# Performance work log

Hardware: AMD Instinct MI355X
Metric: run time of the kernel (lower is better)

The kernel has to match this reference:

```python
import jax, jax.numpy as jnp
import numpy as np

P, N, M, B = 5, 30000, 50000, 256
T, C, L, ED, H, EMB, TD, NL = 13, 16, 3, 4, 128, 64, 5, 3
SRC = jnp.repeat(jnp.arange(P), P)  # edge type i = src*P + dst
DST = jnp.tile(jnp.arange(P), P)


def _affine(x, W, b):
    # x: [P, n, i], W: [P, i, o], b: [P, o]
    return jnp.einsum('pni,pio->pno', x, W) + b[:, None, :]


def _lrelu(x, s=0.01):
    return jnp.where(x >= 0, x, s * x)


def _gat(h, W, a_s, a_d, We, a_e, b, edge_index, edge_attr):
    # h: [P, N, H]; per-edge-type GATConv (heads=1, no self loops) then hetero 'max' aggregation
    hs, hd = h[SRC], h[DST]                       # [25, N, H]
    xl = jnp.einsum('enh,ehf->enf', hs, W)        # transformed source features
    xr = jnp.einsum('enh,ehf->enf', hd, W)
    als = jnp.einsum('enf,ef->en', xl, a_s)
    ald = jnp.einsum('enf,ef->en', xr, a_d)

    def per_type(xl_e, als_e, ald_e, ea, We_e, ae_e, ei):
        src, dst = ei[0], ei[1]
        alpha = als_e[src] + ald_e[dst] + (ea @ We_e) @ ae_e
        alpha = jnp.where(alpha >= 0, alpha, 0.2 * alpha)  # GAT negative_slope=0.2
        amax = jax.ops.segment_max(alpha, dst, num_segments=N)
        ex = jnp.exp(alpha - amax[dst])
        den = jax.ops.segment_sum(ex, dst, num_segments=N)
        w = ex / (den[dst] + 1e-16)
        return jax.ops.segment_sum(w[:, None] * xl_e[src], dst, num_segments=N)

    out = jax.vmap(per_type)(xl, als, ald, edge_attr, We, a_e, edge_index)
    out = out + b[:, None, :]
    return out.reshape(P, P, N, H).max(axis=0)  # HeteroConv aggr='max' over source types


def setup_inputs():
    key = jax.random.key(0)
    ks = iter(jax.random.split(key, 64))
    def nrm(shape, s=1.0):
        return jax.random.normal(next(ks), shape, dtype=jnp.float32) * s
    w = 0.05
    inp = {
        'x': nrm((P, N, T)),
        'cond_x': nrm((P, N, C + L)),
        'edge_attr': nrm((P * P, M, ED)),
        'timesteps': jax.random.uniform(next(ks), (B,), dtype=jnp.float32),
        'te1_W': nrm((1, TD), w), 'te1_b': nrm((TD,), w),
        'te2_W': nrm((TD, TD), w), 'te2_b': nrm((TD,), w),
        'emb_W': nrm((P, T + L, EMB), w), 'emb_b': nrm((P, EMB), w),
        'cemb_W': nrm((P, C, EMB), w), 'cemb_b': nrm((P, EMB), w),
        'pa_W': nrm((P, 2 * EMB, 2 * EMB), w), 'pa_b': nrm((P, 2 * EMB), w),
        'pc_W': nrm((P, 2 * EMB, EMB), w), 'pc_b': nrm((P, EMB), w),
        'sl0_W': nrm((P, EMB + TD, H), w), 'sl0_b': nrm((P, H), w),
        'sl12_W': nrm((2, P, H + TD, H), w), 'sl12_b': nrm((2, P, H), w),
        'slout_W': nrm((P, H + TD, T), w), 'slout_b': nrm((P, T), w),
        'gat_W': nrm((NL, P * P, H, H), w), 'gat_as': nrm((NL, P * P, H), w),
        'gat_ad': nrm((NL, P * P, H), w), 'gat_We': nrm((NL, P * P, ED, H), w),
        'gat_ae': nrm((NL, P * P, H), w), 'gat_b': nrm((NL, P * P, H), w),
        'xc_W': nrm((NL, P, H, H // 2), w), 'xc_b': nrm((NL, P, H // 2), w),
        'cc_W': nrm((NL, P, H, H // 2), w), 'cc_b': nrm((NL, P, H // 2), w),
        'ca_W': nrm((NL, P, H, H), w), 'ca_b': nrm((NL, P, H), w),
        'batch_idx': jax.random.randint(next(ks), (P, N), 0, B),
        'edge_index': jax.random.randint(next(ks), (P * P, 2, M), 0, N),
    }
    return inp


def reference(x, cond_x, edge_attr, timesteps, te1_W, te1_b, te2_W, te2_b,
              emb_W, emb_b, cemb_W, cemb_b, pa_W, pa_b, pc_W, pc_b,
              sl0_W, sl0_b, sl12_W, sl12_b, slout_W, slout_b,
              gat_W, gat_as, gat_ad, gat_We, gat_ae, gat_b,
              xc_W, xc_b, cc_W, cc_b, ca_W, ca_b, batch_idx, edge_index):
    # time embedding: Linear(1,TD) -> SiLU -> Linear(TD,TD)
    temb = jax.nn.silu(timesteps[:, None] @ te1_W + te1_b) @ te2_W + te2_b  # [B, TD]
    cond, latent = cond_x[..., :C], cond_x[..., C:]
    h = _affine(jnp.concatenate([x, latent], -1), emb_W, emb_b)            # [P,N,EMB]
    ce = _affine(cond, cemb_W, cemb_b)
    h = jnp.concatenate([h, ce], -1)                                       # [P,N,2EMB]
    h = jax.nn.sigmoid(_affine(h, pa_W, pa_b)) * h                         # attention pooling
    h = _affine(h, pc_W, pc_b)                                             # [P,N,EMB]
    nt = temb[batch_idx]                                                   # [P,N,TD]
    h = jnp.concatenate([h, nt], -1)
    for l in range(NL):
        if l > 0:
            h = jnp.concatenate([h, nt], -1)
        Wl, bl = (sl0_W, sl0_b) if l == 0 else (sl12_W[l - 1], sl12_b[l - 1])
        h = _lrelu(_affine(h, Wl, bl))                                     # [P,N,H]
        comm = _lrelu(_gat(h, gat_W[l], gat_as[l], gat_ad[l], gat_We[l], gat_ae[l], gat_b[l], edge_index, edge_attr))
        h = jnp.concatenate([_affine(h, xc_W[l], xc_b[l]), _affine(comm, cc_W[l], cc_b[l])], -1)
        h = h + jax.nn.sigmoid(_affine(h, ca_W[l], ca_b[l])) * h
    h = jnp.concatenate([h, nt], -1)
    return _affine(h, slout_W, slout_b)                                    # [P,N,T]
```

## Files before the change

kernel.cpp:

```cpp
#include <hip/hip_runtime.h>
#include <cstdio>

using bf8 = __attribute__((ext_vector_type(8))) short;
using f4v = __attribute__((ext_vector_type(4))) float;
typedef unsigned short u16;
typedef unsigned int u32;

#define DEV __device__ __forceinline__

DEV float bf2f(u16 u){ return __uint_as_float(((u32)u) << 16); }
DEV u16 f2bf(float f){ u32 u = __float_as_uint(f); return (u16)((u + 0x7fffu + ((u >> 16) & 1u)) >> 16); }
DEV float sigm(float v){ return 1.f / (1.f + __expf(-v)); }

constexpr int P5 = 5, NN = 30000, MM = 50000, NE = 25, BB = 256;
constexpr int KC = 96;
constexpr int RS = KC * 2 + 16;

__global__ void temb_k(const float* ts, const float* w1, const float* b1,
                       const float* w2, const float* b2, float* temb){
  int i = blockIdx.x * blockDim.x + threadIdx.x;
  if (i >= BB) return;
  float t = ts[i]; float z[5];
#pragma unroll
  for (int j = 0; j < 5; ++j){ float u = t * w1[j] + b1[j]; z[j] = u * sigm(u); }
#pragma unroll
  for (int j2 = 0; j2 < 5; ++j2){
    float s = b2[j2];
#pragma unroll
    for (int j = 0; j < 5; ++j) s += z[j] * w2[j * 5 + j2];
    temb[i * 5 + j2] = s;
  }
}

__global__ void wtransE_k(const float* __restrict__ W, u16* __restrict__ Wt,
                          int Kreal, int Kpad, int Nreal, int Nalloc, int total){
  int idx = blockIdx.x * blockDim.x + threadIdx.x;
  if (idx >= total) return;
  int k = idx % Kpad;
  int t2 = idx / Kpad;
  int f = t2 % Nalloc;
  int b = t2 / Nalloc;
  float v = (k < Kreal && f < Nreal) ? W[((size_t)b * Kreal + k) * Nreal + f] : 0.f;
  Wt[idx] = f2bf(v);
}

__global__ void embw_k(const float* emb_W, const float* emb_b, const float* cemb_W, const float* cemb_b,
                       u16* Wc, float* bc){
  int b = blockIdx.x, f = threadIdx.x;
  for (int k = 0; k < 32; ++k){
    float v = 0.f;
    if (f < 64){ if (k < 16) v = emb_W[((size_t)b * 16 + k) * 64 + f]; }
    else       { if (k >= 16) v = cemb_W[((size_t)b * 16 + (k - 16)) * 64 + (f - 64)]; }
    Wc[((size_t)b * 128 + f) * 32 + k] = f2bf(v);
  }
  bc[b * 128 + f] = (f < 64) ? emb_b[b * 64 + f] : cemb_b[b * 64 + (f - 64)];
}

__global__ void gwtT_k(const float* __restrict__ gW, u16* __restrict__ gWt){
  int idx = blockIdx.x * blockDim.x + threadIdx.x;
  if (idx >= 75 * 128 * 128) return;
  int h = idx & 127, f = (idx >> 7) & 127, le = idx >> 14;
  gWt[idx] = f2bf(gW[(size_t)le * 16384 + h * 128 + f]);
}

__global__ void gatred_k(const float* gW, const float* gas, const float* gad,
                         const float* gWe, const float* gae,
                         float* wswd, float* eaw){
  int le = blockIdx.x; int h = threadIdx.x;
  const float* W = gW + (size_t)le * 16384;
  const float* as_ = gas + le * 128;
  const float* ad_ = gad + le * 128;
  float wsv = 0.f, wdv = 0.f;
  for (int f = 0; f < 128; ++f){
    float w = W[h * 128 + f];
    wsv += w * as_[f]; wdv += w * ad_[f];
  }
  wswd[le * 256 + h] = wsv;
  wswd[le * 256 + 128 + h] = wdv;
  if (h < 4){
    const float* We = gWe + (size_t)le * 512;
    const float* ae = gae + le * 128;
    float s = 0.f;
    for (int f = 0; f < 128; ++f) s += We[h * 128 + f] * ae[f];
    eaw[le * 4 + h] = s;
  }
}

__global__ void abuild_k(const float* x, const float* cx, u16* A0){
  int idx = blockIdx.x * blockDim.x + threadIdx.x;
  if (idx >= P5 * NN) return;
  const float* xr = x + (size_t)idx * 13;
  const float* cr = cx + (size_t)idx * 19;
  u16* a0 = A0 + (size_t)idx * 32;
#pragma unroll
  for (int i = 0; i < 13; ++i) a0[i] = f2bf(xr[i]);
#pragma unroll
  for (int i = 0; i < 3; ++i) a0[13 + i] = f2bf(cr[16 + i]);
#pragma unroll
  for (int i = 0; i < 16; ++i) a0[16 + i] = f2bf(cr[i]);
}

__global__ void ntfill_k(u16* buf, int pitch, int co, const int* bidx, const float* temb){
  int idx = blockIdx.x * blockDim.x + threadIdx.x;
  if (idx >= P5 * NN) return;
  int b = bidx[idx];
  u16* r = buf + (size_t)idx * pitch;
#pragma unroll
  for (int j = 0; j < 5; ++j) r[co + j] = f2bf(temb[b * 5 + j]);
  for (int j = co + 5; j < pitch; ++j) r[j] = 0;
}

__global__ void csr_count_k(const int* EI, int* cnt){
  int idx = blockIdx.x * blockDim.x + threadIdx.x;
  if (idx >= NE * MM) return;
  int e = idx / MM, m = idx % MM;
  int dst = EI[(size_t)e * 2 * MM + MM + m];
  atomicAdd(&cnt[e * NN + dst], 1);
}

__global__ __launch_bounds__(1024) void csr_scan_k(const int* cnt, int* off){
  int e = blockIdx.x, tid = threadIdx.x;
  int lane = tid & 63, wv = tid >> 6;
  __shared__ int wsum[16];
  int running = 0;
  for (int c = 0; c < 30; ++c){
    int idx = c * 1024 + tid;
    int v = (idx < NN) ? cnt[e * NN + idx] : 0;
    int s = v;
#pragma unroll
    for (int o = 1; o < 64; o <<= 1){
      int t = __shfl_up(s, o, 64);
      if (lane >= o) s += t;
    }
    if (lane == 63) wsum[wv] = s;
    __syncthreads();
    if (wv == 0 && lane < 16){
      int t = wsum[lane];
#pragma unroll
      for (int o = 1; o < 16; o <<= 1){
        int u = __shfl_up(t, o, 64);
        if (lane >= o) t += u;
      }
      wsum[lane] = t;
    }
    __syncthreads();
    int base = running + ((wv > 0) ? wsum[wv - 1] : 0);
    if (idx < NN) off[(size_t)e * (NN + 1) + idx] = base + s - v;
    running += wsum[15];
    __syncthreads();
  }
  if (tid == 0) off[(size_t)e * (NN + 1) + NN] = running;
}

__global__ void csr_fill_k(const int* EI, const int* off, int* cnt, int* mpos){
  int idx = blockIdx.x * blockDim.x + threadIdx.x;
  if (idx >= NE * MM) return;
  int e = idx / MM, m = idx % MM;
  int dst = EI[(size_t)e * 2 * MM + MM + m];
  int pos = off[(size_t)e * (NN + 1) + dst] + atomicAdd(&cnt[e * NN + dst], 1);
  mpos[idx] = pos;
}

__global__ __launch_bounds__(256) void dots2_k(const u16* __restrict__ hS, const float* __restrict__ wswd_l,
                                               float* __restrict__ als, float* __restrict__ ald){
  __shared__ u32 hl[64][65];
  __shared__ float wsl[10][129];
  int p = blockIdx.y;
  int n0 = blockIdx.x * 64;
  int tid = threadIdx.x;
  for (int i = tid; i < 10 * 128; i += 256){
    int col = i >> 7, k = i & 127;
    int e = (col < 5) ? (p * 5 + col) : ((col - 5) * 5 + p);
    wsl[col][k] = wswd_l[e * 256 + ((col < 5) ? 0 : 128) + k];
  }
  for (int i = tid; i < 64 * 64; i += 256){
    int r = i >> 6, kp = i & 63;
    int n = n0 + r;
    hl[r][kp] = (n < NN) ? ((const u32*)hS)[((size_t)p * NN + n) * 64 + kp] : 0u;
  }
  __syncthreads();
  int col = tid & 15, rbase = tid >> 4;
  if (col < 10){
#pragma unroll
    for (int pass = 0; pass < 4; ++pass){
      int r = rbase + pass * 16;
      int n = n0 + r;
      if (n >= NN) continue;
      float s = 0.f;
#pragma unroll
      for (int kp = 0; kp < 64; ++kp){
        u32 pr = hl[r][kp];
        s += bf2f((u16)(pr & 0xffffu)) * wsl[col][2 * kp]
           + bf2f((u16)(pr >> 16)) * wsl[col][2 * kp + 1];
      }
      if (col < 5) als[(size_t)(p * 5 + col) * NN + n] = s;
      else         ald[(size_t)((col - 5) * 5 + p) * NN + n] = s;
    }
  }
}

__global__ __launch_bounds__(256) void alpha_k(const int* EI, const float* ea, const float* als,
                                               const float* ald, const float* eaw_l,
                                               float* alpha, u32* amax){
  int idx = blockIdx.x * blockDim.x + threadIdx.x;
  if (idx >= NE * MM) return;
  int e = idx / MM, m = idx % MM;
  int src = EI[(size_t)e * 2 * MM + m];
  int dst = EI[(size_t)e * 2 * MM + MM + m];
  const float* a4 = ea + ((size_t)e * MM + m) * 4;
  const float* ew = eaw_l + e * 4;
  float a = als[(size_t)e * NN + src] + ald[(size_t)e * NN + dst]
          + a4[0] * ew[0] + a4[1] * ew[1] + a4[2] * ew[2] + a4[3] * ew[3];
  a = (a >= 0.f) ? a : 0.2f * a;
  alpha[(size_t)e * MM + m] = a;
  u32 ua = __float_as_uint(a);
  u32 enc = (ua & 0x80000000u) ? ~ua : (ua | 0x80000000u);
  atomicMax(&amax[(size_t)e * NN + dst], enc);
}

__global__ __launch_bounds__(256) void exprec_k(const int* EI, const float* alpha, const u32* amax,
                                                const int* mpos, uint2* prec){
  int idx = blockIdx.x * blockDim.x + threadIdx.x;
  if (idx >= NE * MM) return;
  int e = idx / MM, m = idx - e * MM;
  int src = EI[(size_t)e * 2 * MM + m];
  int dst = EI[(size_t)e * 2 * MM + MM + m];
  u32 enc = amax[(size_t)e * NN + dst];
  float am = (enc & 0x80000000u) ? __uint_as_float(enc & 0x7fffffffu) : __uint_as_float(~enc);
  float ex = __expf(alpha[idx] - am);
  uint2 pr; pr.x = (u32)src; pr.y = __float_as_uint(ex);
  prec[(size_t)e * MM + mpos[idx]] = pr;
}

__global__ __launch_bounds__(256) void agg3_k(const u16* __restrict__ hS, const uint2* __restrict__ prec,
                                              const int* __restrict__ off, u16* __restrict__ agghB,
                                              int pd0, int npd){
  int l = threadIdx.x & 63, w = threadIdx.x >> 6;
  int n = blockIdx.x * 4 + w;
  if (n >= NN) return;
  int y = blockIdx.y;
  int ps = y / npd, e = ps * 5 + pd0 + (y - ps * npd);
  int ro = off[(size_t)e * (NN + 1) + n], re = off[(size_t)e * (NN + 1) + n + 1];
  const uint2* pe = prec + (size_t)e * MM;
  const u32* hrow = (const u32*)hS + (size_t)ps * NN * 64 + l;
  float den = 0.f, a0 = 0.f, a1 = 0.f;
  for (int j = ro; j < re; ++j){
    uint2 pr = pe[j];
    float ex = __uint_as_float(pr.y);
    u32 hv = hrow[(size_t)pr.x * 64];
    den += ex;
    a0 += ex * bf2f((u16)(hv & 0xffffu));
    a1 += ex * bf2f((u16)(hv >> 16));
  }
  float inv = 1.f / (den + 1e-16f);
  ((u32*)agghB)[((size_t)y * NN + n) * 64 + l] = (u32)f2bf(a0 * inv) | ((u32)f2bf(a1 * inv) << 16);
}

template<int NF, int MI, int NJ, int EPI, bool ALRELU>
__global__ __launch_bounds__(256) void tgemm_k(const u16* __restrict__ A, const u16* __restrict__ Wt,
                                               const float* __restrict__ bias, void* __restrict__ out,
                                               const u16* __restrict__ X,
                                               int Kpad, int opitch, int ocol, int xpitch){
  constexpr int Nalloc = NF * 16;
  constexpr int WR = 128 / (MI * 16);
  constexpr int WC = 4 / WR;
  static_assert(WR * WC == 4 && NJ * WC * 16 == Nalloc, "wave tiling");
  extern __shared__ __align__(16) char smem[];
  float* Cs = (float*)smem;
  const int tid = threadIdx.x;
  const int l = tid & 63, w = tid >> 6;
  const int bz = blockIdx.z;
  const int r0 = blockIdx.x * 128;
  const int wr = w / WC, wc = w % WC;
  const size_t Ab = (size_t)bz * NN;

  f4v acc[MI][NJ];
#pragma unroll
  for (int i = 0; i < MI; ++i)
#pragma unroll
    for (int j = 0; j < NJ; ++j) acc[i][j] = f4v{0.f, 0.f, 0.f, 0.f};

  for (int kb = 0; kb < Kpad; kb += KC){
    int kc = Kpad - kb; if (kc > KC) kc = KC;
    int nseg = kc >> 3;
    for (int s = tid; s < 128 * nseg; s += 256){
      int r = s / nseg, c = s - r * nseg;
      int grow = r0 + r; if (grow > NN - 1) grow = NN - 1;
      uint4 v = *(const uint4*)(A + (Ab + grow) * Kpad + kb + c * 8);
      if (ALRELU){
        u32 pr[4] = {v.x, v.y, v.z, v.w};
#pragma unroll
        for (int q = 0; q < 4; ++q){
          float lo = bf2f((u16)(pr[q] & 0xffffu)), hi = bf2f((u16)(pr[q] >> 16));
          lo = lo >= 0.f ? lo : 0.01f * lo; hi = hi >= 0.f ? hi : 0.01f * hi;
          pr[q] = (u32)f2bf(lo) | ((u32)f2bf(hi) << 16);
        }
        v.x = pr[0]; v.y = pr[1]; v.z = pr[2]; v.w = pr[3];
      }
      *(uint4*)(smem + r * RS + c * 16) = v;
    }
    for (int s = tid; s < Nalloc * nseg; s += 256){
      int r = s / nseg, c = s - r * nseg;
      uint4 v = *(const uint4*)(Wt + ((size_t)bz * Nalloc + r) * Kpad + kb + c * 8);
      *(uint4*)(smem + 128 * RS + r * RS + c * 16) = v;
    }
    __syncthreads();
    int KI = kc >> 5;
    for (int k0 = 0; k0 < KI; ++k0){
      bf8 af[MI], bfr[NJ];
#pragma unroll
      for (int i = 0; i < MI; ++i){
        int row = wr * (MI * 16) + i * 16 + (l & 15);
        af[i] = *(const bf8*)(smem + row * RS + k0 * 64 + (l >> 4) * 16);
      }
#pragma unroll
      for (int j = 0; j < NJ; ++j){
        int col = wc * (NJ * 16) + j * 16 + (l & 15);
        bfr[j] = *(const bf8*)(smem + 128 * RS + col * RS + k0 * 64 + (l >> 4) * 16);
      }
#pragma unroll
      for (int i = 0; i < MI; ++i)
#pragma unroll
        for (int j = 0; j < NJ; ++j)
          acc[i][j] = __builtin_amdgcn_mfma_f32_16x16x32_bf16(af[i], bfr[j], acc[i][j], 0, 0, 0);
    }
    __syncthreads();
  }

  if (EPI == 4){
    int col = l & 15;
    if (col < 13){
#pragma unroll
      for (int i = 0; i < MI; ++i){
        float bv = bias[bz * 13 + col];
#pragma unroll
        for (int r = 0; r < 4; ++r){
          int grow = r0 + wr * (MI * 16) + i * 16 + (l >> 4) * 4 + r;
          if (grow < NN)
            ((float*)out)[((size_t)bz * NN + grow) * 13 + col] = acc[i][0][r] + bv;
        }
      }
    }
    return;
  }

#pragma unroll
  for (int i = 0; i < MI; ++i)
#pragma unroll
    for (int j = 0; j < NJ; ++j){
      int tcol = wc * (NJ * 16) + j * 16 + (l & 15);
      float bv = bias[bz * Nalloc + tcol];
#pragma unroll
      for (int r = 0; r < 4; ++r){
        int trow = wr * (MI * 16) + i * 16 + (l >> 4) * 4 + r;
        float v = acc[i][j][r] + bv;
        if (EPI == 2) v = v >= 0.f ? v : 0.01f * v;
        Cs[trow * Nalloc + tcol] = v;
      }
    }
  __syncthreads();
  constexpr int nsc = Nalloc / 4;
  u16* o16 = (u16*)out;
  for (int s = tid; s < 128 * nsc; s += 256){
    int r = s / nsc, c = s - r * nsc;
    int grow = r0 + r; if (grow >= NN) continue;
    float4 cv = *(const float4*)(Cs + r * Nalloc + c * 4);
    float v0 = cv.x, v1 = cv.y, v2 = cv.z, v3 = cv.w;
    if (EPI == 1 || EPI == 3){
      uint2 xv = *(const uint2*)(X + ((size_t)bz * NN + grow) * xpitch + c * 4);
      float x0 = bf2f((u16)(xv.x & 0xffffu)), x1 = bf2f((u16)(xv.x >> 16));
      float x2 = bf2f((u16)(xv.y & 0xffffu)), x3 = bf2f((u16)(xv.y >> 16));
      if (EPI == 1){ v0 = x0 * sigm(v0); v1 = x1 * sigm(v1); v2 = x2 * sigm(v2); v3 = x3 * sigm(v3); }
      else { v0 = x0 * (1.f + sigm(v0)); v1 = x1 * (1.f + sigm(v1)); v2 = x2 * (1.f + sigm(v2)); v3 = x3 * (1.f + sigm(v3)); }
    }
    uint2 ov;
    ov.x = (u32)f2bf(v0) | ((u32)f2bf(v1) << 16);
    ov.y = (u32)f2bf(v2) | ((u32)f2bf(v3) << 16);
    *(uint2*)(o16 + ((size_t)bz * NN + grow) * opitch + ocol + c * 4) = ov;
  }
}

__global__ __launch_bounds__(256) void tgatmm_k(const u16* __restrict__ agghB, const u16* __restrict__ gWt_l,
                                                const float* __restrict__ gb_l, u16* __restrict__ comm,
                                                int pd, int pd0, int npd){
  extern __shared__ __align__(16) char smem[];
  float* Cs = (float*)smem;
  const int tid = threadIdx.x, l = tid & 63, w = tid >> 6;
  const int r0 = blockIdx.x * 128;
  const int wr = w >> 1, wc = w & 1;
  const int dpd = pd - pd0;
  f4v vmax[4][4];
#pragma unroll
  for (int ps = 0; ps < 5; ++ps){
    int e = ps * 5 + pd;
    const u16* aggs = agghB + (size_t)(ps * npd + dpd) * NN * 128;
    f4v acc[4][4];
#pragma unroll
    for (int i = 0; i < 4; ++i)
#pragma unroll
      for (int j = 0; j < 4; ++j) acc[i][j] = f4v{0.f, 0.f, 0.f, 0.f};
    for (int kb = 0; kb < 128; kb += KC){
      int kc = 128 - kb; if (kc > KC) kc = KC;
      int nseg = kc >> 3;
      for (int s = tid; s < 128 * nseg; s += 256){
        int r = s / nseg, c = s - r * nseg;
        int grow = r0 + r; if (grow > NN - 1) grow = NN - 1;
        uint4 v = *(const uint4*)(aggs + (size_t)grow * 128 + kb + c * 8);
        *(uint4*)(smem + r * RS + c * 16) = v;
      }
      for (int s = tid; s < 128 * nseg; s += 256){
        int r = s / nseg, c = s - r * nseg;
        uint4 v = *(const uint4*)(gWt_l + ((size_t)e * 128 + r) * 128 + kb + c * 8);
        *(uint4*)(smem + 128 * RS + r * RS + c * 16) = v;
      }
      __syncthreads();
      int KI = kc >> 5;
      for (int k0 = 0; k0 < KI; ++k0){
        bf8 af[4], bfr[4];
#pragma unroll
        for (int i = 0; i < 4; ++i){
          int row = wr * 64 + i * 16 + (l & 15);
          af[i] = *(const bf8*)(smem + row * RS + k0 * 64 + (l >> 4) * 16);
        }
#pragma unroll
        for (int j = 0; j < 4; ++j){
          int col = wc * 64 + j * 16 + (l & 15);
          bfr[j] = *(const bf8*)(smem + 128 * RS + col * RS + k0 * 64 + (l >> 4) * 16);
        }
#pragma unroll
        for (int i = 0; i < 4; ++i)
#pragma unroll
          for (int j = 0; j < 4; ++j)
            acc[i][j] = __builtin_amdgcn_mfma_f32_16x16x32_bf16(af[i], bfr[j], acc[i][j], 0, 0, 0);
      }
      __syncthreads();
    }
    const float* be = gb_l + e * 128;
#pragma unroll
    for (int i = 0; i < 4; ++i)
#pragma unroll
      for (int j = 0; j < 4; ++j){
        int tcol = wc * 64 + j * 16 + (l & 15);
        float bv = be[tcol];
#pragma unroll
        for (int r = 0; r < 4; ++r){
          float cvv = acc[i][j][r] + bv;
          vmax[i][j][r] = (ps == 0) ? cvv : fmaxf(vmax[i][j][r], cvv);
        }
      }
  }
#pragma unroll
  for (int i = 0; i < 4; ++i)
#pragma unroll
    for (int j = 0; j < 4; ++j){
      int tcol = wc * 64 + j * 16 + (l & 15);
#pragma unroll
      for (int r = 0; r < 4; ++r){
        int trow = wr * 64 + i * 16 + (l >> 4) * 4 + r;
        Cs[trow * 128 + tcol] = vmax[i][j][r];
      }
    }
  __syncthreads();
  for (int s = tid; s < 128 * 32; s += 256){
    int r = s >> 5, c = s & 31;
    int grow = r0 + r; if (grow >= NN) continue;
    float4 cv = *(const float4*)(Cs + r * 128 + c * 4);
    uint2 ov;
    ov.x = (u32)f2bf(cv.x) | ((u32)f2bf(cv.y) << 16);
    ov.y = (u32)f2bf(cv.z) | ((u32)f2bf(cv.w) << 16);
    *(uint2*)(comm + ((size_t)pd * NN + grow) * 128 + c * 4) = ov;
  }
}

constexpr size_t ALN(size_t x){ return (x + 255) & ~(size_t)255; }
constexpr size_t SZ_A0   = ALN((size_t)P5 * NN * 32 * 2);
constexpr size_t SZ_H0   = ALN((size_t)P5 * NN * 96 * 2);
constexpr size_t SZ_H128 = ALN((size_t)P5 * NN * 128 * 2);
constexpr size_t SZ_HL   = ALN((size_t)P5 * NN * 160 * 2);
constexpr size_t O_A0 = 0;
constexpr size_t O_H0 = O_A0 + SZ_A0;
constexpr size_t O_AGG = 0;
constexpr size_t O_HCAT = O_H0 + SZ_H0;
constexpr size_t O_HG = O_HCAT + SZ_H128;
constexpr size_t O_HS = O_HG + SZ_H128;
constexpr size_t O_HL = O_HS + SZ_H128;
constexpr size_t O_TEMB = O_HL + SZ_HL;
constexpr size_t O_WSWD = O_TEMB + ALN(256 * 5 * 4);
constexpr size_t O_EAW  = O_WSWD + ALN(75 * 256 * 4);
constexpr size_t O_CNT  = O_EAW + ALN(75 * 4 * 4);
constexpr size_t O_OFFS = O_CNT + ALN((size_t)NE * NN * 4);
constexpr size_t O_MPOS = O_OFFS + ALN((size_t)NE * (NN + 1) * 4);
constexpr size_t O_ALS  = O_MPOS + ALN((size_t)NE * MM * 4);
constexpr size_t O_ALD  = O_ALS + ALN((size_t)NE * NN * 4);
constexpr size_t O_ALPHA= O_ALD + ALN((size_t)NE * NN * 4);
constexpr size_t O_AMAX = O_ALPHA + ALN((size_t)NE * MM * 4);
constexpr size_t O_GWT  = O_AMAX + ALN((size_t)NE * NN * 4);
constexpr size_t O_WCMB = O_GWT + ALN((size_t)75 * 16384 * 2);
constexpr size_t O_BCMB = O_WCMB + ALN((size_t)5 * 128 * 32 * 2);
constexpr size_t O_WPA  = O_BCMB + ALN((size_t)5 * 128 * 4);
constexpr size_t O_WPC  = O_WPA + ALN((size_t)5 * 128 * 128 * 2);
constexpr size_t O_WSL0 = O_WPC + ALN((size_t)5 * 64 * 128 * 2);
constexpr size_t O_WSL12= O_WSL0 + ALN((size_t)5 * 128 * 96 * 2);
constexpr size_t O_WSLO = O_WSL12 + ALN((size_t)10 * 128 * 160 * 2);
constexpr size_t O_WXC  = O_WSLO + ALN((size_t)5 * 16 * 160 * 2);
constexpr size_t O_WCC  = O_WXC + ALN((size_t)15 * 64 * 128 * 2);
constexpr size_t O_WCA  = O_WCC + ALN((size_t)15 * 64 * 128 * 2);
constexpr size_t O_PREC = O_WCA + ALN((size_t)15 * 128 * 128 * 2);
constexpr size_t WS_NEED= O_PREC + ALN((size_t)NE * MM * 8);

extern "C" void kernel_launch(void* const* d_in, const int* in_sizes, int n_in,
                              void* d_out, int out_size, void* d_ws, size_t ws_size,
                              hipStream_t stream){
  if (ws_size < WS_NEED){
    fprintf(stderr, "kernel_launch: ws too small: need %zu have %zu\n", WS_NEED, ws_size);
    return;
  }
  const float* x        = (const float*)d_in[0];
  const float* cond_x   = (const float*)d_in[1];
  const float* edge_attr= (const float*)d_in[2];
  const float* timesteps= (const float*)d_in[3];
  const float* te1_W = (const float*)d_in[4];
  const float* te1_b = (const float*)d_in[5];
  const float* te2_W = (const float*)d_in[6];
  const float* te2_b = (const float*)d_in[7];
  const float* emb_W = (const float*)d_in[8];
  const float* emb_b = (const float*)d_in[9];
  const float* cemb_W= (const float*)d_in[10];
  const float* cemb_b= (const float*)d_in[11];
  const float* pa_W  = (const float*)d_in[12];
  const float* pa_b  = (const float*)d_in[13];
  const float* pc_W  = (const float*)d_in[14];
  const float* pc_b  = (const float*)d_in[15];
  const float* sl0_W = (const float*)d_in[16];
  const float* sl0_b = (const float*)d_in[17];
  const float* sl12_W= (const float*)d_in[18];
  const float* sl12_b= (const float*)d_in[19];
  const float* slout_W=(const float*)d_in[20];
  const float* slout_b=(const float*)d_in[21];
  const float* gat_W = (const float*)d_in[22];
  const float* gat_as= (const float*)d_in[23];
  const float* gat_ad= (const float*)d_in[24];
  const float* gat_We= (const float*)d_in[25];
  const float* gat_ae= (const float*)d_in[26];
  const float* gat_b = (const float*)d_in[27];
  const float* xc_W  = (const float*)d_in[28];
  const float* xc_b  = (const float*)d_in[29];
  const float* cc_W  = (const float*)d_in[30];
  const float* cc_b  = (const float*)d_in[31];
  const float* ca_W  = (const float*)d_in[32];
  const float* ca_b  = (const float*)d_in[33];
  const int* batch_idx = (const int*)d_in[34];
  const int* edge_index= (const int*)d_in[35];

  char* ws = (char*)d_ws;
  u16* A0    = (u16*)(ws + O_A0);
  u16* h0buf = (u16*)(ws + O_H0);
  u16* agghB = (u16*)(ws + O_AGG);
  u16* hcat  = (u16*)(ws + O_HCAT);
  u16* hg    = (u16*)(ws + O_HG);
  u16* h2    = (u16*)(ws + O_HG);
  u16* hS    = (u16*)(ws + O_HS);
  u16* hL    = (u16*)(ws + O_HL);
  u16* comm  = (u16*)(ws + O_HL);
  float* tembp = (float*)(ws + O_TEMB);
  float* wswdp = (float*)(ws + O_WSWD);
  float* eawp  = (float*)(ws + O_EAW);
  int* cnt  = (int*)(ws + O_CNT);
  int* offs = (int*)(ws + O_OFFS);
  int* mposp= (int*)(ws + O_MPOS);
  float* alsp = (float*)(ws + O_ALS);
  float* aldp = (float*)(ws + O_ALD);
  float* alphap = (float*)(ws + O_ALPHA);
  u32* amaxp = (u32*)(ws + O_AMAX);
  u16* gwt   = (u16*)(ws + O_GWT);
  u16* wcmb  = (u16*)(ws + O_WCMB);
  float* bcmb= (float*)(ws + O_BCMB);
  u16* wpa   = (u16*)(ws + O_WPA);
  u16* wpc   = (u16*)(ws + O_WPC);
  u16* wsl0  = (u16*)(ws + O_WSL0);
  u16* wsl12 = (u16*)(ws + O_WSL12);
  u16* wslo  = (u16*)(ws + O_WSLO);
  u16* wxc   = (u16*)(ws + O_WXC);
  u16* wcc   = (u16*)(ws + O_WCC);
  u16* wca   = (u16*)(ws + O_WCA);
  uint2* precp = (uint2*)(ws + O_PREC);

  const dim3 B256(256);
  const dim3 TG(235, 1, 5);
  const int GPN = (P5 * NN + 255) / 256;
  const int GEM = (NE * MM + 255) / 256;
  constexpr int LDS_N128 = 65536;
  constexpr int LDS_N64  = 39936;
  constexpr int LDS_SLO  = 29952;

  temb_k<<<1, B256, 0, stream>>>(timesteps, te1_W, te1_b, te2_W, te2_b, tembp);
  embw_k<<<5, 128, 0, stream>>>(emb_W, emb_b, cemb_W, cemb_b, wcmb, bcmb);
  {
    auto WT = [&](const float* W, u16* Wt, int Kr, int Kp, int Nr, int Na, int B){
      int total = B * Na * Kp;
      wtransE_k<<<(total + 255) / 256, B256, 0, stream>>>(W, Wt, Kr, Kp, Nr, Na, total);
    };
    WT(pa_W, wpa, 128, 128, 128, 128, 5);
    WT(pc_W, wpc, 128, 128, 64, 64, 5);
    WT(sl0_W, wsl0, 69, 96, 128, 128, 5);
    WT(sl12_W, wsl12, 133, 160, 128, 128, 10);
    WT(slout_W, wslo, 133, 160, 13, 16, 5);
    WT(xc_W, wxc, 128, 128, 64, 64, 15);
    WT(cc_W, wcc, 128, 128, 64, 64, 15);
    WT(ca_W, wca, 128, 128, 128, 128, 15);
  }
  gwtT_k<<<(75 * 128 * 128 + 255) / 256, B256, 0, stream>>>(gat_W, gwt);
  gatred_k<<<75, 128, 0, stream>>>(gat_W, gat_as, gat_ad, gat_We, gat_ae, wswdp, eawp);

  hipMemsetAsync(cnt, 0, (size_t)NE * NN * 4, stream);
  csr_count_k<<<GEM, B256, 0, stream>>>(edge_index, cnt);
  csr_scan_k<<<25, 1024, 0, stream>>>(cnt, offs);
  hipMemsetAsync(cnt, 0, (size_t)NE * NN * 4, stream);
  csr_fill_k<<<GEM, B256, 0, stream>>>(edge_index, offs, cnt, mposp);

  abuild_k<<<GPN, B256, 0, stream>>>(x, cond_x, A0);
  tgemm_k<8, 4, 4, 0, false><<<TG, B256, LDS_N128, stream>>>(A0, wcmb, bcmb, hcat, nullptr, 32, 128, 0, 0);
  tgemm_k<8, 4, 4, 1, false><<<TG, B256, LDS_N128, stream>>>(hcat, wpa, pa_b, hg, hcat, 128, 128, 0, 128);
  tgemm_k<4, 2, 4, 0, false><<<TG, B256, LDS_N64, stream>>>(hg, wpc, pc_b, h0buf, nullptr, 128, 96, 0, 0);
  ntfill_k<<<GPN, B256, 0, stream>>>(h0buf, 96, 64, batch_idx, tembp);

  for (int l = 0; l < 3; ++l){
    if (l == 0)
      tgemm_k<8, 4, 4, 2, false><<<TG, B256, LDS_N128, stream>>>(h0buf, wsl0, sl0_b, hS, nullptr, 96, 128, 0, 0);
    else
      tgemm_k<8, 4, 4, 2, false><<<TG, B256, LDS_N128, stream>>>(hL, wsl12 + (size_t)(l - 1) * 5 * 128 * 160,
                                                                 sl12_b + (size_t)(l - 1) * 5 * 128, hS, nullptr,
                                                                 160, 128, 0, 0);
    const float* wswd_l = wswdp + (size_t)l * 25 * 256;
    const float* eaw_l = eawp + (size_t)l * 25 * 4;
    const u16* gwt_l = gwt + (size_t)l * 25 * 16384;
    const float* gb_l = gat_b + (size_t)l * 25 * 128;
    dots2_k<<<dim3(469, 5), B256, 0, stream>>>(hS, wswd_l, alsp, aldp);
    hipMemsetAsync(amaxp, 0, (size_t)NE * NN * 4, stream);
    alpha_k<<<GEM, B256, 0, stream>>>(edge_index, edge_attr, alsp, aldp, eaw_l, alphap, amaxp);
    exprec_k<<<GEM, B256, 0, stream>>>(edge_index, alphap, amaxp, mposp, precp);
    agg3_k<<<dim3(7500, 15), B256, 0, stream>>>(hS, precp, offs, agghB, 0, 3);
    for (int pd = 0; pd < 3; ++pd)
      tgatmm_k<<<dim3(235), B256, LDS_N128, stream>>>(agghB, gwt_l, gb_l, comm, pd, 0, 3);
    agg3_k<<<dim3(7500, 10), B256, 0, stream>>>(hS, precp, offs, agghB, 3, 2);
    for (int pd = 3; pd < 5; ++pd)
      tgatmm_k<<<dim3(235), B256, LDS_N128, stream>>>(agghB, gwt_l, gb_l, comm, pd, 3, 2);
    tgemm_k<4, 2, 4, 0, false><<<TG, B256, LDS_N64, stream>>>(hS, wxc + (size_t)l * 5 * 64 * 128,
                                                              xc_b + (size_t)l * 5 * 64, h2, nullptr,
                                                              128, 128, 0, 0);
    tgemm_k<4, 2, 4, 0, true><<<TG, B256, LDS_N64, stream>>>(comm, wcc + (size_t)l * 5 * 64 * 128,
                                                             cc_b + (size_t)l * 5 * 64, h2, nullptr,
                                                             128, 128, 64, 0);
    tgemm_k<8, 4, 4, 3, false><<<TG, B256, LDS_N128, stream>>>(h2, wca + (size_t)l * 5 * 128 * 128,
                                                               ca_b + (size_t)l * 5 * 128, hL, h2,
                                                               128, 160, 0, 128);
    ntfill_k<<<GPN, B256, 0, stream>>>(hL, 160, 128, batch_idx, tembp);
  }

  tgemm_k<1, 2, 1, 4, false><<<TG, B256, LDS_SLO, stream>>>(hL, wslo, slout_b, d_out, nullptr, 160, 13, 0, 0);
}
```

Measured before the change: 2.135 ms.

## Fuse GAT neighbor aggregation with per-edge-type matmul and max reduction

Replaces the separate aggregation kernel (which wrote aggregated bf16 features to a global buffer) and the per-destination-type MFMA matmul kernels with one fused kernel. Each block gathers and softmax-normalizes neighbor features for its 128 destination rows directly into LDS, then runs the MFMA matmul and a running max over source types. This removes the global round-trip of the aggregated features and cuts several launches per layer. In exchange it drops to 1175 blocks, each doing gather-latency-bound work, with 4 rows interleaved per wave to hide latency and with load imbalance from varying degree.

```diff
diff --git a/kernel.cpp b/kernel.cpp
--- a/kernel.cpp
+++ b/kernel.cpp
@@ -15,6 +15,7 @@
 constexpr int P5 = 5, NN = 30000, MM = 50000, NE = 25, BB = 256;
 constexpr int KC = 96;
 constexpr int RS = KC * 2 + 16;
+constexpr int RSA = 272;
 
 __global__ void temb_k(const float* ts, const float* w1, const float* b1,
                        const float* w2, const float* b2, float* temb){
@@ -232,28 +233,122 @@
   prec[(size_t)e * MM + mpos[idx]] = pr;
 }
 
-__global__ __launch_bounds__(256) void agg3_k(const u16* __restrict__ hS, const uint2* __restrict__ prec,
-                                              const int* __restrict__ off, u16* __restrict__ agghB,
-                                              int pd0, int npd){
-  int l = threadIdx.x & 63, w = threadIdx.x >> 6;
-  int n = blockIdx.x * 4 + w;
-  if (n >= NN) return;
-  int y = blockIdx.y;
-  int ps = y / npd, e = ps * 5 + pd0 + (y - ps * npd);
-  int ro = off[(size_t)e * (NN + 1) + n], re = off[(size_t)e * (NN + 1) + n + 1];
-  const uint2* pe = prec + (size_t)e * MM;
-  const u32* hrow = (const u32*)hS + (size_t)ps * NN * 64 + l;
-  float den = 0.f, a0 = 0.f, a1 = 0.f;
-  for (int j = ro; j < re; ++j){
-    uint2 pr = pe[j];
-    float ex = __uint_as_float(pr.y);
-    u32 hv = hrow[(size_t)pr.x * 64];
-    den += ex;
-    a0 += ex * bf2f((u16)(hv & 0xffffu));
-    a1 += ex * bf2f((u16)(hv >> 16));
-  }
-  float inv = 1.f / (den + 1e-16f);
-  ((u32*)agghB)[((size_t)y * NN + n) * 64 + l] = (u32)f2bf(a0 * inv) | ((u32)f2bf(a1 * inv) << 16);
+__global__ __launch_bounds__(256) void fgat_k(const u16* __restrict__ hS, const uint2* __restrict__ prec,
+                                              const int* __restrict__ off, const u16* __restrict__ gWt_l,
+                                              const float* __restrict__ gb_l, u16* __restrict__ comm){
+  extern __shared__ __align__(16) char smem[];
+  char* As = smem;
+  char* Bs = smem + 128 * RSA;
+  float* Cs = (float*)smem;
+  const int tid = threadIdx.x, l = tid & 63, w = tid >> 6;
+  const int pd = blockIdx.y;
+  const int r0 = blockIdx.x * 128;
+  const int wr = w >> 1, wc = w & 1;
+  f4v vmax[4][4];
+#pragma unroll 1
+  for (int ps = 0; ps < 5; ++ps){
+    int e = ps * 5 + pd;
+    {
+      const u16* wb = gWt_l + (size_t)e * 16384;
+      for (int s = tid; s < 128 * 16; s += 256){
+        int r = s >> 4, c = s & 15;
+        *(uint4*)(Bs + r * RSA + c * 16) = *(const uint4*)(wb + r * 128 + c * 8);
+      }
+    }
+    const uint2* pe = prec + (size_t)e * MM;
+    const int* offe = off + (size_t)e * (NN + 1);
+    const u32* hb = (const u32*)hS + (size_t)ps * NN * 64 + l;
+    for (int u = 0; u < 32; u += 4){
+      int rb = w * 32 + u;
+      float den[4] = {0.f, 0.f, 0.f, 0.f};
+      float s0[4] = {0.f, 0.f, 0.f, 0.f};
+      float s1[4] = {0.f, 0.f, 0.f, 0.f};
+      int ro[4], ln[4];
+      int mx = 0;
+#pragma unroll
+      for (int q = 0; q < 4; ++q){
+        int n = r0 + rb + q;
+        if (n < NN){ ro[q] = offe[n]; ln[q] = offe[n + 1] - ro[q]; }
+        else { ro[q] = 0; ln[q] = 0; }
+        mx = (ln[q] > mx) ? ln[q] : mx;
+      }
+      for (int t = 0; t < mx; ++t){
+#pragma unroll
+        for (int q = 0; q < 4; ++q){
+          if (t < ln[q]){
+            uint2 pr = pe[ro[q] + t];
+            float ex = __uint_as_float(pr.y);
+            u32 hv = hb[(size_t)pr.x * 64];
+            den[q] += ex;
+            s0[q] += ex * bf2f((u16)(hv & 0xffffu));
+            s1[q] += ex * bf2f((u16)(hv >> 16));
+          }
+        }
+      }
+#pragma unroll
+      for (int q = 0; q < 4; ++q){
+        float inv = 1.f / (den[q] + 1e-16f);
+        u32 o = (u32)f2bf(s0[q] * inv) | ((u32)f2bf(s1[q] * inv) << 16);
+        *(u32*)(As + (rb + q) * RSA + l * 4) = o;
+      }
+    }
+    __syncthreads();
+    f4v acc[4][4];
+#pragma unroll
+    for (int i = 0; i < 4; ++i)
+#pragma unroll
+      for (int j = 0; j < 4; ++j) acc[i][j] = f4v{0.f, 0.f, 0.f, 0.f};
+#pragma unroll
+    for (int k0 = 0; k0 < 4; ++k0){
+      bf8 af[4], bfr[4];
+#pragma unroll
+      for (int i = 0; i < 4; ++i)
+        af[i] = *(const bf8*)(As + (wr * 64 + i * 16 + (l & 15)) * RSA + k0 * 64 + (l >> 4) * 16);
+#pragma unroll
+      for (int j = 0; j < 4; ++j)
+        bfr[j] = *(const bf8*)(Bs + (wc * 64 + j * 16 + (l & 15)) * RSA + k0 * 64 + (l >> 4) * 16);
+#pragma unroll
+      for (int i = 0; i < 4; ++i)
+#pragma unroll
+        for (int j = 0; j < 4; ++j)
+          acc[i][j] = __builtin_amdgcn_mfma_f32_16x16x32_bf16(af[i], bfr[j], acc[i][j], 0, 0, 0);
+    }
+    const float* be = gb_l + e * 128;
+#pragma unroll
+    for (int i = 0; i < 4; ++i)
+#pragma unroll
+      for (int j = 0; j < 4; ++j){
+        int tcol = wc * 64 + j * 16 + (l & 15);
+        float bv = be[tcol];
+#pragma unroll
+        for (int r = 0; r < 4; ++r){
+          float cvv = acc[i][j][r] + bv;
+          vmax[i][j][r] = (ps == 0) ? cvv : fmaxf(vmax[i][j][r], cvv);
+        }
+      }
+    __syncthreads();
+  }
+#pragma unroll
+  for (int i = 0; i < 4; ++i)
+#pragma unroll
+    for (int j = 0; j < 4; ++j){
+      int tcol = wc * 64 + j * 16 + (l & 15);
+#pragma unroll
+      for (int r = 0; r < 4; ++r){
+        int trow = wr * 64 + i * 16 + (l >> 4) * 4 + r;
+        Cs[trow * 128 + tcol] = vmax[i][j][r];
+      }
+    }
+  __syncthreads();
+  for (int s = tid; s < 128 * 32; s += 256){
+    int r = s >> 5, c = s & 31;
+    int grow = r0 + r; if (grow >= NN) continue;
+    float4 cv = *(const float4*)(Cs + r * 128 + c * 4);
+    uint2 ov;
+    ov.x = (u32)f2bf(cv.x) | ((u32)f2bf(cv.y) << 16);
+    ov.y = (u32)f2bf(cv.z) | ((u32)f2bf(cv.w) << 16);
+    *(uint2*)(comm + ((size_t)pd * NN + grow) * 128 + c * 4) = ov;
+  }
 }
 
 template<int NF, int MI, int NJ, int EPI, bool ALRELU>
@@ -380,98 +475,6 @@
   }
 }
 
-__global__ __launch_bounds__(256) void tgatmm_k(const u16* __restrict__ agghB, const u16* __restrict__ gWt_l,
-                                                const float* __restrict__ gb_l, u16* __restrict__ comm,
-                                                int pd, int pd0, int npd){
-  extern __shared__ __align__(16) char smem[];
-  float* Cs = (float*)smem;
-  const int tid = threadIdx.x, l = tid & 63, w = tid >> 6;
-  const int r0 = blockIdx.x * 128;
-  const int wr = w >> 1, wc = w & 1;
-  const int dpd = pd - pd0;
-  f4v vmax[4][4];
-#pragma unroll
-  for (int ps = 0; ps < 5; ++ps){
-    int e = ps * 5 + pd;
-    const u16* aggs = agghB + (size_t)(ps * npd + dpd) * NN * 128;
-    f4v acc[4][4];
-#pragma unroll
-    for (int i = 0; i < 4; ++i)
-#pragma unroll
-      for (int j = 0; j < 4; ++j) acc[i][j] = f4v{0.f, 0.f, 0.f, 0.f};
-    for (int kb = 0; kb < 128; kb += KC){
-      int kc = 128 - kb; if (kc > KC) kc = KC;
-      int nseg = kc >> 3;
-      for (int s = tid; s < 128 * nseg; s += 256){
-        int r = s / nseg, c = s - r * nseg;
-        int grow = r0 + r; if (grow > NN - 1) grow = NN - 1;
-        uint4 v = *(const uint4*)(aggs + (size_t)grow * 128 + kb + c * 8);
-        *(uint4*)(smem + r * RS + c * 16) = v;
-      }
-      for (int s = tid; s < 128 * nseg; s += 256){
-        int r = s / nseg, c = s - r * nseg;
-        uint4 v = *(const uint4*)(gWt_l + ((size_t)e * 128 + r) * 128 + kb + c * 8);
-        *(uint4*)(smem + 128 * RS + r * RS + c * 16) = v;
-      }
-      __syncthreads();
-      int KI = kc >> 5;
-      for (int k0 = 0; k0 < KI; ++k0){
-        bf8 af[4], bfr[4];
-#pragma unroll
-        for (int i = 0; i < 4; ++i){
-          int row = wr * 64 + i * 16 + (l & 15);
-          af[i] = *(const bf8*)(smem + row * RS + k0 * 64 + (l >> 4) * 16);
-        }
-#pragma unroll
-        for (int j = 0; j < 4; ++j){
-          int col = wc * 64 + j * 16 + (l & 15);
-          bfr[j] = *(const bf8*)(smem + 128 * RS + col * RS + k0 * 64 + (l >> 4) * 16);
-        }
-#pragma unroll
-        for (int i = 0; i < 4; ++i)
-#pragma unroll
-          for (int j = 0; j < 4; ++j)
-            acc[i][j] = __builtin_amdgcn_mfma_f32_16x16x32_bf16(af[i], bfr[j], acc[i][j], 0, 0, 0);
-      }
-      __syncthreads();
-    }
-    const float* be = gb_l + e * 128;
-#pragma unroll
-    for (int i = 0; i < 4; ++i)
-#pragma unroll
-      for (int j = 0; j < 4; ++j){
-        int tcol = wc * 64 + j * 16 + (l & 15);
-        float bv = be[tcol];
-#pragma unroll
-        for (int r = 0; r < 4; ++r){
-          float cvv = acc[i][j][r] + bv;
-          vmax[i][j][r] = (ps == 0) ? cvv : fmaxf(vmax[i][j][r], cvv);
-        }
-      }
-  }
-#pragma unroll
-  for (int i = 0; i < 4; ++i)
-#pragma unroll
-    for (int j = 0; j < 4; ++j){
-      int tcol = wc * 64 + j * 16 + (l & 15);
-#pragma unroll
-      for (int r = 0; r < 4; ++r){
-        int trow = wr * 64 + i * 16 + (l >> 4) * 4 + r;
-        Cs[trow * 128 + tcol] = vmax[i][j][r];
-      }
-    }
-  __syncthreads();
-  for (int s = tid; s < 128 * 32; s += 256){
-    int r = s >> 5, c = s & 31;
-    int grow = r0 + r; if (grow >= NN) continue;
-    float4 cv = *(const float4*)(Cs + r * 128 + c * 4);
-    uint2 ov;
-    ov.x = (u32)f2bf(cv.x) | ((u32)f2bf(cv.y) << 16);
-    ov.y = (u32)f2bf(cv.z) | ((u32)f2bf(cv.w) << 16);
-    *(uint2*)(comm + ((size_t)pd * NN + grow) * 128 + c * 4) = ov;
-  }
-}
-
 constexpr size_t ALN(size_t x){ return (x + 255) & ~(size_t)255; }
 constexpr size_t SZ_A0   = ALN((size_t)P5 * NN * 32 * 2);
 constexpr size_t SZ_H0   = ALN((size_t)P5 * NN * 96 * 2);
@@ -479,7 +482,6 @@
 constexpr size_t SZ_HL   = ALN((size_t)P5 * NN * 160 * 2);
 constexpr size_t O_A0 = 0;
 constexpr size_t O_H0 = O_A0 + SZ_A0;
-constexpr size_t O_AGG = 0;
 constexpr size_t O_HCAT = O_H0 + SZ_H0;
 constexpr size_t O_HG = O_HCAT + SZ_H128;
 constexpr size_t O_HS = O_HG + SZ_H128;
@@ -555,7 +557,6 @@
   char* ws = (char*)d_ws;
   u16* A0    = (u16*)(ws + O_A0);
   u16* h0buf = (u16*)(ws + O_H0);
-  u16* agghB = (u16*)(ws + O_AGG);
   u16* hcat  = (u16*)(ws + O_HCAT);
   u16* hg    = (u16*)(ws + O_HG);
   u16* h2    = (u16*)(ws + O_HG);
@@ -592,6 +593,7 @@
   constexpr int LDS_N128 = 65536;
   constexpr int LDS_N64  = 39936;
   constexpr int LDS_SLO  = 29952;
+  constexpr int LDS_FGAT = 128 * RSA * 2;
 
   temb_k<<<1, B256, 0, stream>>>(timesteps, te1_W, te1_b, te2_W, te2_b, tembp);
   embw_k<<<5, 128, 0, stream>>>(emb_W, emb_b, cemb_W, cemb_b, wcmb, bcmb);
@@ -639,12 +641,7 @@
     hipMemsetAsync(amaxp, 0, (size_t)NE * NN * 4, stream);
     alpha_k<<<GEM, B256, 0, stream>>>(edge_index, edge_attr, alsp, aldp, eaw_l, alphap, amaxp);
     exprec_k<<<GEM, B256, 0, stream>>>(edge_index, alphap, amaxp, mposp, precp);
-    agg3_k<<<dim3(7500, 15), B256, 0, stream>>>(hS, precp, offs, agghB, 0, 3);
-    for (int pd = 0; pd < 3; ++pd)
-      tgatmm_k<<<dim3(235), B256, LDS_N128, stream>>>(agghB, gwt_l, gb_l, comm, pd, 0, 3);
-    agg3_k<<<dim3(7500, 10), B256, 0, stream>>>(hS, precp, offs, agghB, 3, 2);
-    for (int pd = 3; pd < 5; ++pd)
-      tgatmm_k<<<dim3(235), B256, LDS_N128, stream>>>(agghB, gwt_l, gb_l, comm, pd, 3, 2);
+    fgat_k<<<dim3(235, 5), B256, LDS_FGAT, stream>>>(hS, precp, offs, gwt_l, gb_l, comm);
     tgemm_k<4, 2, 4, 0, false><<<TG, B256, LDS_N64, stream>>>(hS, wxc + (size_t)l * 5 * 64 * 128,
                                                               xc_b + (size_t)l * 5 * 64, h2, nullptr,
                                                               128, 128, 0, 0);
```

Result: slower. 3.883 ms (+81.9%).
